# Kernel tuning notes

Hardware: AMD Instinct MI355X
Metric: run time of the kernel (lower is better)

## Reference

```python
import jax, jax.numpy as jnp
import numpy as np

B, N, DIN, DOUT = 8, 2048, 512, 256
NUM_BUCKETS = 20


def setup_inputs() -> dict:
    key = jax.random.key(0)
    ks = jax.random.split(key, 12)
    s_in = 1.0 / np.sqrt(DIN)
    s_out = 1.0 / np.sqrt(DOUT)
    return {
        "x": jax.random.normal(ks[0], (B, N, DIN), dtype=jnp.float32),
        "price_rank": jax.random.randint(ks[1], (B, N), 0, N, dtype=jnp.int64),
        "Wq": jax.random.uniform(ks[2], (DOUT, DIN), jnp.float32, -s_in, s_in),
        "bq": jax.random.uniform(ks[3], (DOUT,), jnp.float32, -s_in, s_in),
        "Wk": jax.random.uniform(ks[4], (DOUT, DIN), jnp.float32, -s_in, s_in),
        "bk": jax.random.uniform(ks[5], (DOUT,), jnp.float32, -s_in, s_in),
        "Wv": jax.random.uniform(ks[6], (DOUT, DIN), jnp.float32, -s_in, s_in),
        "bv": jax.random.uniform(ks[7], (DOUT,), jnp.float32, -s_in, s_in),
        "Ws": jax.random.uniform(ks[8], (1, DOUT), jnp.float32, -s_out, s_out),
        "bs": jax.random.uniform(ks[9], (1,), jnp.float32, -s_out, s_out),
        "rank_emb": jax.random.normal(ks[10], (NUM_BUCKETS, 1), dtype=jnp.float32),
        "rank_w": jnp.ones((1,), dtype=jnp.float32),
    }


def reference(x, price_rank, Wq, bq, Wk, bk, Wv, bv, Ws, bs, rank_emb, rank_w):
    scale = jnp.sqrt(jnp.asarray(DOUT, dtype=x.dtype))
    q = jnp.einsum("bnd,od->bno", x, Wq) + bq  # [B,N,DOUT]
    k = jnp.einsum("bnd,od->bno", x, Wk) + bk
    v = jnp.einsum("bnd,od->bno", x, Wv) + bv
    scores = jnp.einsum("bno,bmo->bnm", q, k) / scale  # [B,N,N]
    # learned pairwise rank-distance bias gate
    rank_dist = jnp.abs(price_rank[:, :, None] - price_rank[:, None, :])
    buckets = jnp.clip(rank_dist // 5, 0, NUM_BUCKETS - 1)  # [B,N,N] int
    prior = rank_emb[buckets, 0]  # gather embedding, squeeze last dim
    gate = jax.nn.sigmoid(rank_w[0] * prior)
    scores = scores * gate
    attn = jax.nn.softmax(scores, axis=2)
    context = jnp.einsum("bnm,bmo->bno", attn, v)  # [B,N,DOUT]
    winner = jax.nn.sigmoid(jnp.einsum("bno,uo->bnu", context, Ws) + bs)[..., 0]
    return winner  # [B,N]
```

## Files before the change

kernel.cpp:

```cpp
#include <hip/hip_runtime.h>
#include <hip/hip_bf16.h>

#define B_    8
#define N_    2048
#define DIN_  512
#define DOUT_ 256
#define NBUCK 20

typedef __attribute__((ext_vector_type(8))) short  short8;
typedef __attribute__((ext_vector_type(4))) float  floatx4;

__device__ __forceinline__ unsigned short f2b(float f) {
    __hip_bfloat16 h = __float2bfloat16(f);
    unsigned short u;
    __builtin_memcpy(&u, &h, 2);
    return u;
}

__device__ __forceinline__ void load_lds16(const unsigned short* g, unsigned short* l) {
    __builtin_amdgcn_global_load_lds(
        (const __attribute__((address_space(1))) unsigned int*)g,
        (__attribute__((address_space(3))) unsigned int*)l, 16, 0, 0);
}

__device__ __forceinline__ float fexp2(float x) {
    float r;
    asm("v_exp_f32 %0, %1" : "=v"(r) : "v"(x));
    return r;
}

__global__ __launch_bounds__(256) void prep_kernel(
    const float* __restrict__ Wv, const float* __restrict__ Ws,
    const float* __restrict__ bv,
    float* __restrict__ wvs, float* __restrict__ bvs) {
    const int blk = blockIdx.x, tid = threadIdx.x;
    __shared__ float wsl[DOUT_];
    wsl[tid] = Ws[tid];
    __syncthreads();
    if (tid < 128) {
        int d = blk * 128 + tid;
        float s0 = 0.f, s1 = 0.f, s2 = 0.f, s3 = 0.f;
#pragma unroll 8
        for (int o = 0; o < DOUT_; o += 4) {
            s0 += Wv[(size_t)(o + 0) * DIN_ + d] * wsl[o + 0];
            s1 += Wv[(size_t)(o + 1) * DIN_ + d] * wsl[o + 1];
            s2 += Wv[(size_t)(o + 2) * DIN_ + d] * wsl[o + 2];
            s3 += Wv[(size_t)(o + 3) * DIN_ + d] * wsl[o + 3];
        }
        wvs[d] = (s0 + s1) + (s2 + s3);
    }
    if (blk == 0 && tid < 64) {
        float bb = wsl[tid] * bv[tid] + wsl[tid + 64] * bv[tid + 64] +
                   wsl[tid + 128] * bv[tid + 128] + wsl[tid + 192] * bv[tid + 192];
        for (int off = 1; off < 64; off <<= 1) bb += __shfl_xor(bb, off, 64);
        if (tid == 0) *bvs = bb;
    }
}

__global__ __launch_bounds__(256) void cvt_x_kernel(const float* __restrict__ x,
                                                    const float* __restrict__ wvs,
                                                    const float* __restrict__ bvs,
                                                    const float* __restrict__ wq,
                                                    const float* __restrict__ wk,
                                                    unsigned short* __restrict__ xb,
                                                    unsigned short* __restrict__ wdst,
                                                    float* __restrict__ vw) {
    int tid = threadIdx.x;
    if (blockIdx.x >= 4096) {
        int i = ((blockIdx.x - 4096) * 256 + tid) * 8;
        const float* src = (i < 131072) ? (wq + i) : (wk + (i - 131072));
        float4 a = *(const float4*)(src);
        float4 b = *(const float4*)(src + 4);
        uint4 r;
        r.x = f2b(a.x) | ((unsigned)f2b(a.y) << 16);
        r.y = f2b(a.z) | ((unsigned)f2b(a.w) << 16);
        r.z = f2b(b.x) | ((unsigned)f2b(b.y) << 16);
        r.w = f2b(b.z) | ((unsigned)f2b(b.w) << 16);
        *(uint4*)(wdst + i) = r;
        return;
    }
    int wave = tid >> 6, lane = tid & 63;
    int row = blockIdx.x * 4 + wave;
    size_t base = (size_t)row * DIN_ + lane * 8;
    float4 a = *(const float4*)(x + base);
    float4 b = *(const float4*)(x + base + 4);
    float4 wa = *(const float4*)(wvs + lane * 8);
    float4 wb = *(const float4*)(wvs + lane * 8 + 4);
    uint4 r;
    r.x = f2b(a.x) | ((unsigned)f2b(a.y) << 16);
    r.y = f2b(a.z) | ((unsigned)f2b(a.w) << 16);
    r.z = f2b(b.x) | ((unsigned)f2b(b.y) << 16);
    r.w = f2b(b.z) | ((unsigned)f2b(b.w) << 16);
    *(uint4*)(xb + base) = r;
    float d = a.x * wa.x + a.y * wa.y + a.z * wa.z + a.w * wa.w +
              b.x * wb.x + b.y * wb.y + b.z * wb.z + b.w * wb.w;
    for (int off = 1; off < 64; off <<= 1) d += __shfl_xor(d, off, 64);
    if (lane == 0) vw[row] = d + *bvs;
}

__global__ __launch_bounds__(256, 2) void qkv_kernel(
    const unsigned short* __restrict__ xb, const unsigned short* __restrict__ wb,
    const float* __restrict__ bq, const float* __restrict__ bk,
    unsigned short* __restrict__ qo, unsigned short* __restrict__ ko) {
    __shared__ unsigned short alds[2][128 * 64];
    __shared__ unsigned short blds[2][128 * 64];
    const int g = blockIdx.x;
    const int xcd = g & 7, t2 = g >> 3;
    const int colBlk = t2 & 3, rowGrp = t2 >> 2;
    const int rowBlk = rowGrp * 8 + xcd;
    const int tid = threadIdx.x;
    const int wave = tid >> 6, lane = tid & 63, quad = lane >> 4, l16 = lane & 15;
    const int wr = wave >> 1, wc = wave & 1;
    const int row0 = rowBlk * 128, col0 = colBlk * 128;
    const int sw3 = l16 & 7;

    floatx4 acc[4][4];
#pragma unroll
    for (int i = 0; i < 4; ++i)
#pragma unroll
        for (int j = 0; j < 4; ++j) acc[i][j] = (floatx4){0.f, 0.f, 0.f, 0.f};

    const int gseg = (lane & 7) ^ (lane >> 3);
    const unsigned short* ag = xb + (size_t)(row0 + wave * 8 + (lane >> 3)) * DIN_ + gseg * 8;
    const unsigned short* bg = wb + (size_t)(col0 + wave * 8 + (lane >> 3)) * DIN_ + gseg * 8;

#pragma unroll
    for (int i = 0; i < 4; ++i) {
        load_lds16(ag + (size_t)i * 32 * DIN_, &alds[0][wave * 512 + i * 2048]);
        load_lds16(bg + (size_t)i * 32 * DIN_, &blds[0][wave * 512 + i * 2048]);
    }
    __syncthreads();

#pragma unroll 1
    for (int t = 0; t < 8; ++t) {
        const unsigned short* al = (t & 1) ? alds[1] : alds[0];
        const unsigned short* bl = (t & 1) ? blds[1] : blds[0];
        unsigned short* aln = (t & 1) ? &alds[0][0] : &alds[1][0];
        unsigned short* bln = (t & 1) ? &blds[0][0] : &blds[1][0];
        if (t < 7) {
            size_t koff = (size_t)(t + 1) * 64;
#pragma unroll
            for (int i = 0; i < 4; ++i) {
                load_lds16(ag + (size_t)i * 32 * DIN_ + koff, aln + wave * 512 + i * 2048);
                load_lds16(bg + (size_t)i * 32 * DIN_ + koff, bln + wave * 512 + i * 2048);
            }
        }
#pragma unroll
        for (int h = 0; h < 2; ++h) {
            short8 af[4], bf[4];
#pragma unroll
            for (int f = 0; f < 4; ++f) {
                int ar = wr * 64 + f * 16 + l16;
                int br = wc * 64 + f * 16 + l16;
                int s  = (h * 4 + quad) ^ sw3;
                af[f] = *(const short8*)&al[(size_t)ar * 64 + s * 8];
                bf[f] = *(const short8*)&bl[(size_t)br * 64 + s * 8];
            }
#pragma unroll
            for (int i = 0; i < 4; ++i)
#pragma unroll
                for (int j = 0; j < 4; ++j)
                    acc[i][j] = __builtin_amdgcn_mfma_f32_16x16x32_bf16(af[i], bf[j], acc[i][j], 0, 0, 0);
        }
        __syncthreads();
    }

#pragma unroll
    for (int j = 0; j < 4; ++j) {
        int col = col0 + wc * 64 + j * 16 + l16;
        unsigned short* dst = (col < 256) ? qo : ko;
        float bias = (col < 256) ? bq[col] : bk[col - 256];
        int c = col & 255;
#pragma unroll
        for (int i = 0; i < 4; ++i)
#pragma unroll
            for (int r = 0; r < 4; ++r) {
                int row = row0 + wr * 64 + i * 16 + quad * 4 + r;
                dst[(size_t)row * DOUT_ + c] = f2b(acc[i][j][r] + bias);
            }
    }
}

__global__ __launch_bounds__(512, 2) void attn_kernel(
    const unsigned short* __restrict__ q, const unsigned short* __restrict__ k,
    const float* __restrict__ vw, const int* __restrict__ pr,
    const float* __restrict__ rank_emb, const float* __restrict__ rank_w,
    const float* __restrict__ bs, float* __restrict__ out) {
    const int g = blockIdx.x;
    const int b = g & 7, rblk = g >> 3;
    const int tid = threadIdx.x, wave = tid >> 6, lane = tid & 63;
    const int quad = lane >> 4, l16 = lane & 15;
    const int n0 = rblk * 64;
    const int rg = wave >> 2, ch = wave & 3;

    __shared__ unsigned short kbuf[2][32768];
    __shared__ float gtab_r[NBUCK * 8];
    __shared__ float lL[8][32], wdL[8][32];

    if (tid < NBUCK * 8)
        gtab_r[tid] = 0.0625f * 1.44269504f /
                      (1.f + __expf(-rank_w[0] * rank_emb[tid >> 3]));

    const unsigned short* qb = q + (size_t)b * N_ * DOUT_;
    const unsigned short* kb = k + (size_t)b * N_ * DOUT_;
    const float* vwb = vw + b * N_;
    const int* prb = pr + b * N_;
    const int l8 = lane & 7;

    short8 qf[2][8];
#pragma unroll
    for (int a = 0; a < 2; ++a)
#pragma unroll
        for (int c = 0; c < 8; ++c)
            qf[a][c] = *(const short8*)(qb + (size_t)(n0 + rg * 32 + a * 16 + l16) * DOUT_ + c * 32 + quad * 8);

    float prn5[2][4];
#pragma unroll
    for (int a = 0; a < 2; ++a)
#pragma unroll
        for (int r = 0; r < 4; ++r)
            prn5[a][r] = (float)prb[n0 + rg * 32 + a * 16 + quad * 4 + r] * 0.2f;

    float lacc[2][4], wacc[2][4];
#pragma unroll
    for (int a = 0; a < 2; ++a)
#pragma unroll
        for (int r = 0; r < 4; ++r) { lacc[a][r] = 0.f; wacc[a][r] = 0.f; }

    const int stg_rbase = wave * 2 + (lane >> 5);
    const int stg_gseg  = (lane & 31) ^ (stg_rbase & 7);
    const unsigned short* stg_src0 = kb + (size_t)stg_rbase * DOUT_ + stg_gseg * 8;
    unsigned short* sdst0 = &kbuf[0][wave * 512];
    unsigned short* sdst1 = &kbuf[1][wave * 512];

    auto stage = [&](int j, unsigned short* sdst) {
        const unsigned short* src = stg_src0 + (size_t)j * 128 * DOUT_;
#pragma unroll
        for (int i = 0; i < 8; ++i)
            load_lds16(src + (size_t)i * 4096, sdst + i * 4096);
    };
    auto mfma = [&](floatx4 (&s)[2][2], const unsigned short* buf) {
#pragma unroll
        for (int a = 0; a < 2; ++a)
#pragma unroll
            for (int cf = 0; cf < 2; ++cf) s[a][cf] = (floatx4){0.f, 0.f, 0.f, 0.f};
        __builtin_amdgcn_s_setprio(1);
#pragma unroll
        for (int c = 0; c < 8; ++c) {
            int seg = (c * 4 + quad) ^ l8;
            short8 kf0 = *(const short8*)&buf[(size_t)(ch * 32 + l16) * 256 + seg * 8];
            short8 kf1 = *(const short8*)&buf[(size_t)(ch * 32 + 16 + l16) * 256 + seg * 8];
            s[0][0] = __builtin_amdgcn_mfma_f32_16x16x32_bf16(qf[0][c], kf0, s[0][0], 0, 0, 0);
            s[1][0] = __builtin_amdgcn_mfma_f32_16x16x32_bf16(qf[1][c], kf0, s[1][0], 0, 0, 0);
            s[0][1] = __builtin_amdgcn_mfma_f32_16x16x32_bf16(qf[0][c], kf1, s[0][1], 0, 0, 0);
            s[1][1] = __builtin_amdgcn_mfma_f32_16x16x32_bf16(qf[1][c], kf1, s[1][1], 0, 0, 0);
        }
        __builtin_amdgcn_s_setprio(0);
    };
    auto gate = [&](floatx4 (&s)[2][2], int pm0, int pm1, float w0, float w1) {
        float pm5_0 = (float)pm0 * 0.2f, pm5_1 = (float)pm1 * 0.2f;
#pragma unroll
        for (int a = 0; a < 2; ++a)
#pragma unroll
            for (int r = 0; r < 4; ++r) {
                float d0 = fabsf(prn5[a][r] - pm5_0);
                int i0 = (int)fminf(d0, 19.0f);
                float p0 = fexp2(s[a][0][r] * gtab_r[i0 * 8 + l8]);
                lacc[a][r] += p0;
                wacc[a][r] += p0 * w0;
                float d1 = fabsf(prn5[a][r] - pm5_1);
                int i1 = (int)fminf(d1, 19.0f);
                float p1 = fexp2(s[a][1][r] * gtab_r[i1 * 8 + l8]);
                lacc[a][r] += p1;
                wacc[a][r] += p1 * w1;
            }
    };

    floatx4 sA[2][2], sB[2][2];
    const int colq = ch * 32 + l16;

    stage(0, sdst0);
    int   pmA0 = prb[colq], pmA1 = prb[colq + 16];
    float wA0 = vwb[colq], wA1 = vwb[colq + 16];
    __syncthreads();
    stage(1, sdst1);
    int   pmB0 = prb[128 + colq], pmB1 = prb[128 + colq + 16];
    float wB0 = vwb[128 + colq], wB1 = vwb[128 + colq + 16];
    mfma(sA, kbuf[0]);
    __syncthreads();

#pragma unroll 1
    for (int jj = 0; jj < 7; ++jj) {
        {
            int jn = 2 * jj + 2;
            stage(jn, sdst0);
            int   p0 = prb[jn * 128 + colq], p1 = prb[jn * 128 + colq + 16];
            float w0 = vwb[jn * 128 + colq], w1 = vwb[jn * 128 + colq + 16];
            mfma(sB, kbuf[1]);
            __builtin_amdgcn_sched_barrier(0);
            gate(sA, pmA0, pmA1, wA0, wA1);
            pmA0 = p0; pmA1 = p1; wA0 = w0; wA1 = w1;
            __syncthreads();
        }
        {
            int jn = 2 * jj + 3;
            stage(jn, sdst1);
            int   p0 = prb[jn * 128 + colq], p1 = prb[jn * 128 + colq + 16];
            float w0 = vwb[jn * 128 + colq], w1 = vwb[jn * 128 + colq + 16];
            mfma(sA, kbuf[0]);
            __builtin_amdgcn_sched_barrier(0);
            gate(sB, pmB0, pmB1, wB0, wB1);
            pmB0 = p0; pmB1 = p1; wB0 = w0; wB1 = w1;
            __syncthreads();
        }
    }
    mfma(sB, kbuf[1]);
    __builtin_amdgcn_sched_barrier(0);
    gate(sA, pmA0, pmA1, wA0, wA1);
    gate(sB, pmB0, pmB1, wB0, wB1);

#pragma unroll
    for (int off = 1; off < 16; off <<= 1) {
#pragma unroll
        for (int a = 0; a < 2; ++a)
#pragma unroll
            for (int r = 0; r < 4; ++r) {
                lacc[a][r] += __shfl_xor(lacc[a][r], off, 64);
                wacc[a][r] += __shfl_xor(wacc[a][r], off, 64);
            }
    }
    if (l16 == 0) {
#pragma unroll
        for (int a = 0; a < 2; ++a)
#pragma unroll
            for (int r = 0; r < 4; ++r) {
                int row = a * 16 + quad * 4 + r;
                lL[wave][row]  = lacc[a][r];
                wdL[wave][row] = wacc[a][r];
            }
    }
    __syncthreads();
    if (tid < 64) {
        int rg2 = tid >> 5, sub = tid & 31;
        float l = 0.f, wd = 0.f;
#pragma unroll
        for (int c2 = 0; c2 < 4; ++c2) {
            l  += lL[rg2 * 4 + c2][sub];
            wd += wdL[rg2 * 4 + c2][sub];
        }
        float logit = wd / l + bs[0];
        out[(size_t)b * N_ + n0 + tid] = 1.f / (1.f + __expf(-logit));
    }
}

extern "C" void kernel_launch(void* const* d_in, const int* in_sizes, int n_in,
                              void* d_out, int out_size, void* d_ws, size_t ws_size,
                              hipStream_t stream) {
    const float* x   = (const float*)d_in[0];
    const int*   pr  = (const int*)d_in[1];
    const float* Wq  = (const float*)d_in[2];
    const float* bq  = (const float*)d_in[3];
    const float* Wk  = (const float*)d_in[4];
    const float* bk  = (const float*)d_in[5];
    const float* Wv  = (const float*)d_in[6];
    const float* bv  = (const float*)d_in[7];
    const float* Ws  = (const float*)d_in[8];
    const float* bs  = (const float*)d_in[9];
    const float* remb = (const float*)d_in[10];
    const float* rw   = (const float*)d_in[11];
    float* out = (float*)d_out;

    char* ws = (char*)d_ws;
    unsigned short* xb  = (unsigned short*)ws;
    unsigned short* wb  = (unsigned short*)(ws + 16777216);
    unsigned short* q   = (unsigned short*)(ws + 17301504);
    unsigned short* kk  = (unsigned short*)(ws + 25690112);
    float*          vwp = (float*)(ws + 34078720);
    float*          wvs = (float*)(ws + 34144256);
    float*          bvs = (float*)(ws + 34146304);

    hipLaunchKernelGGL(prep_kernel, dim3(4), dim3(256), 0, stream,
                       Wv, Ws, bv, wvs, bvs);
    hipLaunchKernelGGL(cvt_x_kernel, dim3(4224), dim3(256), 0, stream,
                       x, wvs, bvs, Wq, Wk, xb, wb, vwp);
    hipLaunchKernelGGL(qkv_kernel, dim3(512), dim3(256), 0, stream,
                       xb, wb, bq, bk, q, kk);
    hipLaunchKernelGGL(attn_kernel, dim3(256), dim3(512), 0, stream,
                       q, kk, vwp, pr, remb, rw, bs, out);
}
```

Baseline: 147.9 us.

## Remap attention waves to cover all 64 query rows over 16 key columns

Each of the 8 waves now holds Q fragments for all 64 rows of the block and processes a distinct 16-column slice of every 128-key tile, instead of a 32-row by 32-column sub-tile. This halves the K LDS reads per wave per tile and simplifies the per-column rank/value loads and the final reduction, at the cost of doubling Q fragment and accumulator registers. Launch bounds are relaxed to one block per CU to accommodate the higher register pressure, which can reduce occupancy and latency hiding.

After: 167.2 us. +13.0%, slower.

```diff
diff --git a/kernel.cpp b/kernel.cpp
--- a/kernel.cpp
+++ b/kernel.cpp
@@ -181,7 +181,7 @@
     }
 }
 
-__global__ __launch_bounds__(512, 2) void attn_kernel(
+__global__ __launch_bounds__(512, 1) void attn_kernel(
     const unsigned short* __restrict__ q, const unsigned short* __restrict__ k,
     const float* __restrict__ vw, const int* __restrict__ pr,
     const float* __restrict__ rank_emb, const float* __restrict__ rank_w,
@@ -191,11 +191,11 @@
     const int tid = threadIdx.x, wave = tid >> 6, lane = tid & 63;
     const int quad = lane >> 4, l16 = lane & 15;
     const int n0 = rblk * 64;
-    const int rg = wave >> 2, ch = wave & 3;
+    const int l8 = lane & 7;
 
     __shared__ unsigned short kbuf[2][32768];
     __shared__ float gtab_r[NBUCK * 8];
-    __shared__ float lL[8][32], wdL[8][32];
+    __shared__ float lL[8][64], wdL[8][64];
 
     if (tid < NBUCK * 8)
         gtab_r[tid] = 0.0625f * 1.44269504f /
@@ -205,25 +205,24 @@
     const unsigned short* kb = k + (size_t)b * N_ * DOUT_;
     const float* vwb = vw + b * N_;
     const int* prb = pr + b * N_;
-    const int l8 = lane & 7;
-
-    short8 qf[2][8];
-#pragma unroll
-    for (int a = 0; a < 2; ++a)
+
+    short8 qf[4][8];
+#pragma unroll
+    for (int a = 0; a < 4; ++a)
 #pragma unroll
         for (int c = 0; c < 8; ++c)
-            qf[a][c] = *(const short8*)(qb + (size_t)(n0 + rg * 32 + a * 16 + l16) * DOUT_ + c * 32 + quad * 8);
-
-    float prn5[2][4];
-#pragma unroll
-    for (int a = 0; a < 2; ++a)
+            qf[a][c] = *(const short8*)(qb + (size_t)(n0 + a * 16 + l16) * DOUT_ + c * 32 + quad * 8);
+
+    float prn5[4][4];
+#pragma unroll
+    for (int a = 0; a < 4; ++a)
 #pragma unroll
         for (int r = 0; r < 4; ++r)
-            prn5[a][r] = (float)prb[n0 + rg * 32 + a * 16 + quad * 4 + r] * 0.2f;
-
-    float lacc[2][4], wacc[2][4];
-#pragma unroll
-    for (int a = 0; a < 2; ++a)
+            prn5[a][r] = (float)prb[n0 + a * 16 + quad * 4 + r] * 0.2f;
+
+    float lacc[4][4], wacc[4][4];
+#pragma unroll
+    for (int a = 0; a < 4; ++a)
 #pragma unroll
         for (int r = 0; r < 4; ++r) { lacc[a][r] = 0.f; wacc[a][r] = 0.f; }
 
@@ -239,53 +238,45 @@
         for (int i = 0; i < 8; ++i)
             load_lds16(src + (size_t)i * 4096, sdst + i * 4096);
     };
-    auto mfma = [&](floatx4 (&s)[2][2], const unsigned short* buf) {
-#pragma unroll
-        for (int a = 0; a < 2; ++a)
-#pragma unroll
-            for (int cf = 0; cf < 2; ++cf) s[a][cf] = (floatx4){0.f, 0.f, 0.f, 0.f};
+    auto mfma = [&](floatx4 (&s)[4], const unsigned short* buf) {
+#pragma unroll
+        for (int a = 0; a < 4; ++a) s[a] = (floatx4){0.f, 0.f, 0.f, 0.f};
         __builtin_amdgcn_s_setprio(1);
 #pragma unroll
         for (int c = 0; c < 8; ++c) {
             int seg = (c * 4 + quad) ^ l8;
-            short8 kf0 = *(const short8*)&buf[(size_t)(ch * 32 + l16) * 256 + seg * 8];
-            short8 kf1 = *(const short8*)&buf[(size_t)(ch * 32 + 16 + l16) * 256 + seg * 8];
-            s[0][0] = __builtin_amdgcn_mfma_f32_16x16x32_bf16(qf[0][c], kf0, s[0][0], 0, 0, 0);
-            s[1][0] = __builtin_amdgcn_mfma_f32_16x16x32_bf16(qf[1][c], kf0, s[1][0], 0, 0, 0);
-            s[0][1] = __builtin_amdgcn_mfma_f32_16x16x32_bf16(qf[0][c], kf1, s[0][1], 0, 0, 0);
-            s[1][1] = __builtin_amdgcn_mfma_f32_16x16x32_bf16(qf[1][c], kf1, s[1][1], 0, 0, 0);
+            short8 kf = *(const short8*)&buf[(size_t)(wave * 16 + l16) * 256 + seg * 8];
+            s[0] = __builtin_amdgcn_mfma_f32_16x16x32_bf16(qf[0][c], kf, s[0], 0, 0, 0);
+            s[1] = __builtin_amdgcn_mfma_f32_16x16x32_bf16(qf[1][c], kf, s[1], 0, 0, 0);
+            s[2] = __builtin_amdgcn_mfma_f32_16x16x32_bf16(qf[2][c], kf, s[2], 0, 0, 0);
+            s[3] = __builtin_amdgcn_mfma_f32_16x16x32_bf16(qf[3][c], kf, s[3], 0, 0, 0);
         }
         __builtin_amdgcn_s_setprio(0);
     };
-    auto gate = [&](floatx4 (&s)[2][2], int pm0, int pm1, float w0, float w1) {
-        float pm5_0 = (float)pm0 * 0.2f, pm5_1 = (float)pm1 * 0.2f;
-#pragma unroll
-        for (int a = 0; a < 2; ++a)
+    auto gate = [&](floatx4 (&s)[4], int pm, float w) {
+        float pm5 = (float)pm * 0.2f;
+#pragma unroll
+        for (int a = 0; a < 4; ++a)
 #pragma unroll
             for (int r = 0; r < 4; ++r) {
-                float d0 = fabsf(prn5[a][r] - pm5_0);
-                int i0 = (int)fminf(d0, 19.0f);
-                float p0 = fexp2(s[a][0][r] * gtab_r[i0 * 8 + l8]);
-                lacc[a][r] += p0;
-                wacc[a][r] += p0 * w0;
-                float d1 = fabsf(prn5[a][r] - pm5_1);
-                int i1 = (int)fminf(d1, 19.0f);
-                float p1 = fexp2(s[a][1][r] * gtab_r[i1 * 8 + l8]);
-                lacc[a][r] += p1;
-                wacc[a][r] += p1 * w1;
+                float d = fabsf(prn5[a][r] - pm5);
+                int idx = (int)fminf(d, 19.0f);
+                float p = fexp2(s[a][r] * gtab_r[idx * 8 + l8]);
+                lacc[a][r] += p;
+                wacc[a][r] += p * w;
             }
     };
 
-    floatx4 sA[2][2], sB[2][2];
-    const int colq = ch * 32 + l16;
+    floatx4 sA[4], sB[4];
+    const int colq = wave * 16 + l16;
 
     stage(0, sdst0);
-    int   pmA0 = prb[colq], pmA1 = prb[colq + 16];
-    float wA0 = vwb[colq], wA1 = vwb[colq + 16];
+    int   pmA = prb[colq];
+    float wA  = vwb[colq];
     __syncthreads();
     stage(1, sdst1);
-    int   pmB0 = prb[128 + colq], pmB1 = prb[128 + colq + 16];
-    float wB0 = vwb[128 + colq], wB1 = vwb[128 + colq + 16];
+    int   pmB = prb[128 + colq];
+    float wB  = vwb[128 + colq];
     mfma(sA, kbuf[0]);
     __syncthreads();
 
@@ -294,35 +285,35 @@
         {
             int jn = 2 * jj + 2;
             stage(jn, sdst0);
-            int   p0 = prb[jn * 128 + colq], p1 = prb[jn * 128 + colq + 16];
-            float w0 = vwb[jn * 128 + colq], w1 = vwb[jn * 128 + colq + 16];
+            int   p0 = prb[jn * 128 + colq];
+            float w0 = vwb[jn * 128 + colq];
             mfma(sB, kbuf[1]);
             __builtin_amdgcn_sched_barrier(0);
-            gate(sA, pmA0, pmA1, wA0, wA1);
-            pmA0 = p0; pmA1 = p1; wA0 = w0; wA1 = w1;
+            gate(sA, pmA, wA);
+            pmA = p0; wA = w0;
             __syncthreads();
         }
         {
             int jn = 2 * jj + 3;
             stage(jn, sdst1);
-            int   p0 = prb[jn * 128 + colq], p1 = prb[jn * 128 + colq + 16];
-            float w0 = vwb[jn * 128 + colq], w1 = vwb[jn * 128 + colq + 16];
+            int   p0 = prb[jn * 128 + colq];
+            float w0 = vwb[jn * 128 + colq];
             mfma(sA, kbuf[0]);
             __builtin_amdgcn_sched_barrier(0);
-            gate(sB, pmB0, pmB1, wB0, wB1);
-            pmB0 = p0; pmB1 = p1; wB0 = w0; wB1 = w1;
+            gate(sB, pmB, wB);
+            pmB = p0; wB = w0;
             __syncthreads();
         }
     }
     mfma(sB, kbuf[1]);
     __builtin_amdgcn_sched_barrier(0);
-    gate(sA, pmA0, pmA1, wA0, wA1);
-    gate(sB, pmB0, pmB1, wB0, wB1);
+    gate(sA, pmA, wA);
+    gate(sB, pmB, wB);
 
 #pragma unroll
     for (int off = 1; off < 16; off <<= 1) {
 #pragma unroll
-        for (int a = 0; a < 2; ++a)
+        for (int a = 0; a < 4; ++a)
 #pragma unroll
             for (int r = 0; r < 4; ++r) {
                 lacc[a][r] += __shfl_xor(lacc[a][r], off, 64);
@@ -331,7 +322,7 @@
     }
     if (l16 == 0) {
 #pragma unroll
-        for (int a = 0; a < 2; ++a)
+        for (int a = 0; a < 4; ++a)
 #pragma unroll
             for (int r = 0; r < 4; ++r) {
                 int row = a * 16 + quad * 4 + r;
@@ -341,13 +332,9 @@
     }
     __syncthreads();
     if (tid < 64) {
-        int rg2 = tid >> 5, sub = tid & 31;
         float l = 0.f, wd = 0.f;
 #pragma unroll
-        for (int c2 = 0; c2 < 4; ++c2) {
-            l  += lL[rg2 * 4 + c2][sub];
-            wd += wdL[rg2 * 4 + c2][sub];
-        }
+        for (int s2 = 0; s2 < 8; ++s2) { l += lL[s2][tid]; wd += wdL[s2][tid]; }
         float logit = wd / l + bs[0];
         out[(size_t)b * N_ + n0 + tid] = 1.f / (1.f + __expf(-logit));
     }
```
